# Kernel tuning notes

Measured on AMD Instinct MI355X. Metric: run time of the kernel, lower is better.

The kernel has to match this reference:

```python
import jax, jax.numpy as jnp
import numpy as np
import math

N_QUBITS = 8
N_QLAYERS = 1
LN_EPS = 1e-5


def _rx(state, theta, wire, n):
    # state: (N, 2,...,2) complex64 with n qubit axes; theta: (N,)
    sh = (theta.shape[0],) + (1,) * (n - 1)
    c = jnp.cos(theta / 2).reshape(sh)
    s = jnp.sin(theta / 2).reshape(sh)
    a = jax.lax.index_in_dim(state, 0, wire + 1, keepdims=False)
    b = jax.lax.index_in_dim(state, 1, wire + 1, keepdims=False)
    return jnp.stack([c * a - 1j * s * b, -1j * s * a + c * b], axis=wire + 1)


def _cnot(state, cw, tw, n):
    s0 = jax.lax.index_in_dim(state, 0, cw + 1, keepdims=False)
    s1 = jax.lax.index_in_dim(state, 1, cw + 1, keepdims=False)
    t_ax = tw + 1 if tw < cw else tw  # target axis index after removing control axis
    s1 = jnp.flip(s1, axis=t_ax)
    return jnp.stack([s0, s1], axis=cw + 1)


def _quantum(angles, qweights):
    # AngleEmbedding (RX) + BasicEntanglerLayers (RX + CNOT ring) + PauliZ expvals
    # angles: (N, 8) float; qweights: (1, 8) float -> returns (N, 8) float
    n = N_QUBITS
    N = angles.shape[0]
    state = jnp.zeros((N,) + (2,) * n, jnp.complex64)
    state = state.at[(slice(None),) + (0,) * n].set(1.0 + 0j)
    for w in range(n):
        state = _rx(state, angles[:, w], w, n)
    for l in range(N_QLAYERS):
        for w in range(n):
            state = _rx(state, jnp.broadcast_to(qweights[l, w], (N,)), w, n)
        for cw in range(n):
            state = _cnot(state, cw, (cw + 1) % n, n)
    probs = state.real ** 2 + state.imag ** 2
    zs = []
    for w in range(n):
        p = probs.sum(axis=tuple(a for a in range(1, n + 1) if a != w + 1))  # (N, 2)
        zs.append(p[:, 0] - p[:, 1])
    return jnp.stack(zs, axis=-1)


def _layernorm(x, g, b):
    m = x.mean(-1, keepdims=True)
    v = ((x - m) ** 2).mean(-1, keepdims=True)
    return (x - m) / jnp.sqrt(v + LN_EPS) * g + b


def _forward(x, Wq, Wk, Wv, Wo, ln1_g, ln1_b, W1, b1, W2, b2, ln2_g, ln2_b,
             ql1_w, ql1_b, qweights, ql2_w, ql2_b):
    B, S, D = x.shape
    H = 16
    dk = D // H
    q = (x @ Wq.T).reshape(B, S, H, dk)
    k = (x @ Wk.T).reshape(B, S, H, dk)
    v = (x @ Wv.T).reshape(B, S, H, dk)
    scores = jnp.einsum('bqhd,bkhd->bhqk', q, k) * (1.0 / math.sqrt(dk))
    attn = jax.nn.softmax(scores, axis=-1)
    o = jnp.einsum('bhqk,bkhd->bqhd', attn, v).reshape(B, S, D) @ Wo.T
    x = _layernorm(o + x, ln1_g, ln1_b)
    ff = jax.nn.relu(x @ W1.T + b1) @ W2.T + b2
    x = _layernorm(ff + x, ln2_g, ln2_b)
    angles = (x @ ql1_w.T + ql1_b).reshape(B * S, N_QUBITS)
    z = _quantum(angles, qweights).reshape(B, S, N_QUBITS).astype(x.dtype)
    y = jnp.concatenate([z, x], axis=2) @ ql2_w.T + ql2_b
    return y


def setup_inputs() -> dict:
    key = jax.random.key(0)
    ks = jax.random.split(key, 12)
    B, S, D, F = 4, 1024, 1024, 4096
    sc = 0.02
    w = lambda k, *sh: jax.random.normal(k, sh, jnp.float32) * sc
    return {
        'x': jax.random.normal(ks[0], (B, S, D), jnp.float32),
        'Wq': w(ks[1], D, D), 'Wk': w(ks[2], D, D), 'Wv': w(ks[3], D, D), 'Wo': w(ks[4], D, D),
        'ln1_g': jnp.ones((D,), jnp.float32), 'ln1_b': jnp.zeros((D,), jnp.float32),
        'W1': w(ks[5], F, D), 'b1': jnp.zeros((F,), jnp.float32),
        'W2': w(ks[6], D, F), 'b2': jnp.zeros((D,), jnp.float32),
        'ln2_g': jnp.ones((D,), jnp.float32), 'ln2_b': jnp.zeros((D,), jnp.float32),
        'ql1_w': w(ks[7], N_QUBITS, D), 'ql1_b': jnp.zeros((N_QUBITS,), jnp.float32),
        'qweights': jax.random.uniform(ks[8], (N_QLAYERS, N_QUBITS), jnp.float32, 0.0, 2 * np.pi),
        'ql2_w': w(ks[9], D, D + N_QUBITS), 'ql2_b': jnp.zeros((D,), jnp.float32),
    }


def reference(x, Wq, Wk, Wv, Wo, ln1_g, ln1_b, W1, b1, W2, b2, ln2_g, ln2_b,
              ql1_w, ql1_b, qweights, ql2_w, ql2_b):
    return _forward(x, Wq, Wk, Wv, Wo, ln1_g, ln1_b, W1, b1, W2, b2, ln2_g, ln2_b,
                    ql1_w, ql1_b, qweights, ql2_w, ql2_b)
```

## Files before the change

kernel.cpp:

```cpp
#include <hip/hip_runtime.h>
#include <hip/hip_bf16.h>

typedef __bf16 bf16_t;
typedef __attribute__((ext_vector_type(8))) __bf16 bf16x8;
typedef __attribute__((ext_vector_type(4))) float floatx4;

#define BM 128

enum { EPI_NONE = 0, EPI_RESID, EPI_BIAS_RELU, EPI_BIAS_RESID, EPI_QL2, EPI_PART };

__device__ __forceinline__ void gld_lds16(const bf16_t* g, bf16_t* l) {
  __builtin_amdgcn_global_load_lds(
      (__attribute__((address_space(1))) void*)(g),
      (__attribute__((address_space(3))) void*)(l), 16, 0, 0);
}

template<int ROWS, int COLS>
__device__ __forceinline__ void stage_swz(const bf16_t* g, int ld, bf16_t* lds, int tid) {
  constexpr int G = COLS / 8;
  #pragma unroll
  for (int i = 0; i < ROWS * G / 256; ++i) {
    int ci = i * 256 + tid;
    int row = ci / G, cc = ci % G;
    int gg = (G == 8) ? (cc ^ (row & 7)) : ((cc & 8) | ((cc & 7) ^ (row & 7)));
    gld_lds16(g + (size_t)row * ld + gg * 8, lds + ci * 8);
  }
}

__device__ __forceinline__ void core128(const bf16_t* __restrict__ Ag,
                                        const bf16_t* __restrict__ Bg,
                                        int Kloop, int lda, int ldb,
                                        bf16_t* As, bf16_t* Bs,
                                        floatx4 acc[4][4]) {
  const int tid = threadIdx.x;
  const int wid = tid >> 6, lane = tid & 63;
  const int wm = (wid >> 1) * 64, wn = (wid & 1) * 64;
  const int m16 = lane & 15, quad = lane >> 4;
  const int r7 = m16 & 7;
  for (int k0 = 0; k0 < Kloop; k0 += 64) {
    stage_swz<128, 64>(Ag + k0, lda, As, tid);
    stage_swz<128, 64>(Bg + k0, ldb, Bs, tid);
    __syncthreads();
    #pragma unroll
    for (int ks = 0; ks < 2; ++ks) {
      const int gi = ks * 4 + quad;
      const int slot = gi ^ r7;
      bf16x8 af[4], bfr[4];
      #pragma unroll
      for (int mt = 0; mt < 4; ++mt)
        af[mt] = *(const bf16x8*)&As[((wm + mt * 16 + m16) * 8 + slot) * 8];
      #pragma unroll
      for (int nt = 0; nt < 4; ++nt)
        bfr[nt] = *(const bf16x8*)&Bs[((wn + nt * 16 + m16) * 8 + slot) * 8];
      #pragma unroll
      for (int mt = 0; mt < 4; ++mt)
        #pragma unroll
        for (int nt = 0; nt < 4; ++nt)
          acc[mt][nt] = __builtin_amdgcn_mfma_f32_16x16x32_bf16(af[mt], bfr[nt], acc[mt][nt], 0, 0, 0);
    }
    __syncthreads();
  }
}

template<int EPI>
__global__ __launch_bounds__(256)
void gemm128(const bf16_t* __restrict__ A, const bf16_t* __restrict__ B,
             bf16_t* __restrict__ C, const float* __restrict__ bias,
             int N, int K) {
  __shared__ bf16_t As[BM * 64];
  __shared__ bf16_t Bs[BM * 64];
  const int tid = threadIdx.x;
  const int wid = tid >> 6, lane = tid & 63;
  const int wm = (wid >> 1) * 64, wn = (wid & 1) * 64;
  const int m16 = lane & 15, quad = lane >> 4;
  const int m0 = blockIdx.y * BM, n0 = blockIdx.x * BM;
  floatx4 acc[4][4];
  const floatx4 vzero = {0.f, 0.f, 0.f, 0.f};
  #pragma unroll
  for (int mt = 0; mt < 4; ++mt)
    #pragma unroll
    for (int nt = 0; nt < 4; ++nt) acc[mt][nt] = vzero;
  core128(A + (size_t)m0 * K, B + (size_t)n0 * K, K, K, K, As, Bs, acc);
  #pragma unroll
  for (int mt = 0; mt < 4; ++mt)
    #pragma unroll
    for (int nt = 0; nt < 4; ++nt) {
      const int gcol = n0 + wn + nt * 16 + m16;
      float bv = (EPI == EPI_BIAS_RELU) ? bias[gcol] : 0.f;
      #pragma unroll
      for (int r = 0; r < 4; ++r) {
        const int grow = m0 + wm + mt * 16 + quad * 4 + r;
        float v = acc[mt][nt][r];
        if (EPI == EPI_BIAS_RELU) { v += bv; v = fmaxf(v, 0.f); }
        C[(size_t)grow * N + gcol] = (bf16_t)v;
      }
    }
}

__global__ __launch_bounds__(256)
void gemm128_sk(const bf16_t* __restrict__ A, const bf16_t* __restrict__ B,
                bf16_t* __restrict__ p0, bf16_t* __restrict__ p1,
                int N, int K, int ldb, int mblocks, int nblocks) {
  __shared__ bf16_t As[BM * 64];
  __shared__ bf16_t Bs[BM * 64];
  const int tid = threadIdx.x;
  const int wid = tid >> 6, lane = tid & 63;
  const int wm = (wid >> 1) * 64, wn = (wid & 1) * 64;
  const int m16 = lane & 15, quad = lane >> 4;
  const int id = blockIdx.x;
  const int m0 = (id % mblocks) * BM;
  const int rest = id / mblocks;
  const int n0 = (rest % nblocks) * BM;
  const int kh = rest / nblocks;
  const int Keff = K / 2;
  floatx4 acc[4][4];
  const floatx4 vzero = {0.f, 0.f, 0.f, 0.f};
  #pragma unroll
  for (int mt = 0; mt < 4; ++mt)
    #pragma unroll
    for (int nt = 0; nt < 4; ++nt) acc[mt][nt] = vzero;
  core128(A + (size_t)m0 * K + (size_t)kh * Keff,
          B + (size_t)n0 * ldb + (size_t)kh * Keff, Keff, K, ldb, As, Bs, acc);
  bf16_t* Cp = kh ? p1 : p0;
  #pragma unroll
  for (int mt = 0; mt < 4; ++mt)
    #pragma unroll
    for (int nt = 0; nt < 4; ++nt) {
      const int gcol = n0 + wn + nt * 16 + m16;
      #pragma unroll
      for (int r = 0; r < 4; ++r) {
        const int grow = m0 + wm + mt * 16 + quad * 4 + r;
        Cp[(size_t)grow * N + gcol] = (bf16_t)acc[mt][nt][r];
      }
    }
}

__global__ __launch_bounds__(256)
void gemm_qkv(const bf16_t* __restrict__ X, const bf16_t* __restrict__ Wb,
              bf16_t* __restrict__ Qo, bf16_t* __restrict__ Ko, bf16_t* __restrict__ Vt) {
  __shared__ bf16_t As[BM * 64];
  __shared__ bf16_t Bs[BM * 64];
  const int tid = threadIdx.x;
  const int wid = tid >> 6, lane = tid & 63;
  const int wm = (wid >> 1) * 64, wn = (wid & 1) * 64;
  const int m16 = lane & 15, quad = lane >> 4;
  const int m0 = blockIdx.y * BM, n0 = blockIdx.x * BM;
  const int sel = blockIdx.z;
  const bf16_t* B = Wb + (size_t)sel * 1024 * 1024;
  floatx4 acc[4][4];
  const floatx4 vzero = {0.f, 0.f, 0.f, 0.f};
  #pragma unroll
  for (int mt = 0; mt < 4; ++mt)
    #pragma unroll
    for (int nt = 0; nt < 4; ++nt) acc[mt][nt] = vzero;
  core128(X + (size_t)m0 * 1024, B + (size_t)n0 * 1024, 1024, 1024, 1024, As, Bs, acc);
  if (sel < 2) {
    bf16_t* C = sel ? Ko : Qo;
    const float sc = sel ? 1.f : 0.125f;
    #pragma unroll
    for (int mt = 0; mt < 4; ++mt)
      #pragma unroll
      for (int nt = 0; nt < 4; ++nt) {
        const int gcol = n0 + wn + nt * 16 + m16;
        #pragma unroll
        for (int r = 0; r < 4; ++r) {
          const int grow = m0 + wm + mt * 16 + quad * 4 + r;
          C[(size_t)grow * 1024 + gcol] = (bf16_t)(acc[mt][nt][r] * sc);
        }
      }
  } else {
    #pragma unroll
    for (int mt = 0; mt < 4; ++mt) {
      const int grow0 = m0 + wm + mt * 16 + quad * 4;
      const int b = grow0 >> 10, s = grow0 & 1023;
      #pragma unroll
      for (int nt = 0; nt < 4; ++nt) {
        const int gcol = n0 + wn + nt * 16 + m16;
        const int h = gcol >> 6, d = gcol & 63;
        #pragma unroll
        for (int r = 0; r < 4; ++r)
          Vt[(((size_t)b * 16 + h) * 64 + d) * 1024 + s + r] = (bf16_t)acc[mt][nt][r];
      }
    }
  }
}

template<int EPI, bool OUTF32>
__global__ __launch_bounds__(256)
void gemm64(const bf16_t* __restrict__ A, const bf16_t* __restrict__ B,
            void* __restrict__ Cv,
            const bf16_t* __restrict__ resid, const float* __restrict__ bias,
            const bf16_t* __restrict__ z, const float* __restrict__ zw,
            int N, int K, int ldb, int boff, int mblocks) {
  __shared__ bf16_t As[BM * 128];
  __shared__ bf16_t Bs[64 * 128];
  const int tid = threadIdx.x;
  const int wid = tid >> 6, lane = tid & 63;
  const int wm = (wid >> 1) * 64, wn = (wid & 1) * 32;
  const int m16 = lane & 15, quad = lane >> 4;
  const int r7 = m16 & 7;
  const int id = blockIdx.x;
  const int m0 = (id % mblocks) * BM, n0 = (id / mblocks) * 64;
  const bf16_t* Ag = A + (size_t)m0 * K;
  const bf16_t* Bg = B + (size_t)n0 * ldb + boff;
  floatx4 acc[4][2];
  const floatx4 vzero = {0.f, 0.f, 0.f, 0.f};
  #pragma unroll
  for (int mt = 0; mt < 4; ++mt)
    #pragma unroll
    for (int nt = 0; nt < 2; ++nt) acc[mt][nt] = vzero;
  for (int k0 = 0; k0 < K; k0 += 128) {
    stage_swz<128, 128>(Ag + k0, K, As, tid);
    stage_swz<64, 128>(Bg + k0, ldb, Bs, tid);
    __syncthreads();
    #pragma unroll
    for (int ks = 0; ks < 4; ++ks) {
      const int gi = ks * 4 + quad;
      const int slot = (gi & 8) | ((gi & 7) ^ r7);
      bf16x8 af[4], bfr[2];
      #pragma unroll
      for (int mt = 0; mt < 4; ++mt)
        af[mt] = *(const bf16x8*)&As[((wm + mt * 16 + m16) * 16 + slot) * 8];
      #pragma unroll
      for (int nt = 0; nt < 2; ++nt)
        bfr[nt] = *(const bf16x8*)&Bs[((wn + nt * 16 + m16) * 16 + slot) * 8];
      #pragma unroll
      for (int mt = 0; mt < 4; ++mt)
        #pragma unroll
        for (int nt = 0; nt < 2; ++nt)
          acc[mt][nt] = __builtin_amdgcn_mfma_f32_16x16x32_bf16(af[mt], bfr[nt], acc[mt][nt], 0, 0, 0);
    }
    __syncthreads();
  }
  #pragma unroll
  for (int mt = 0; mt < 4; ++mt)
    #pragma unroll
    for (int nt = 0; nt < 2; ++nt) {
      const int gcol = n0 + wn + nt * 16 + m16;
      float bv = 0.f;
      if (EPI == EPI_QL2) bv = bias[gcol];
      #pragma unroll
      for (int r = 0; r < 4; ++r) {
        const int grow = m0 + wm + mt * 16 + quad * 4 + r;
        float v = acc[mt][nt][r];
        if (EPI == EPI_RESID) v += (float)resid[(size_t)grow * N + gcol];
        if (EPI == EPI_QL2) {
          float s = 0.f;
          #pragma unroll
          for (int u = 0; u < 8; ++u)
            s += (float)z[(size_t)grow * 8 + u] * zw[(size_t)gcol * 1032 + u];
          v += bv + s;
        }
        if (OUTF32) ((float*)Cv)[(size_t)grow * N + gcol] = v;
        else        ((bf16_t*)Cv)[(size_t)grow * N + gcol] = (bf16_t)v;
      }
    }
}

__global__ __launch_bounds__(256)
void attn_kernel(const bf16_t* __restrict__ Q, const bf16_t* __restrict__ Kb,
                 const bf16_t* __restrict__ Vt, bf16_t* __restrict__ O) {
  __shared__ bf16_t Qs[64 * 64];
  __shared__ bf16_t Ks[128 * 64];
  __shared__ bf16_t Vs[64 * 128];
  __shared__ bf16_t Ps[4][16 * 128];
  const int tid = threadIdx.x;
  const int wid = tid >> 6, lane = tid & 63;
  const int m16 = lane & 15, quad = lane >> 4;
  const int qt = blockIdx.x, bh = blockIdx.y;
  const int b = bh >> 4, h = bh & 15;
  const size_t qbase = ((size_t)(b * 1024 + qt * 64)) * 1024 + h * 64;
  #pragma unroll
  for (int i = 0; i < 2; ++i) {
    int ci = i * 256 + tid;
    int row = ci >> 3, cc = ci & 7;
    *(bf16x8*)&Qs[row * 64 + ((cc ^ (row & 7)) * 8)] =
        *(const bf16x8*)&Q[qbase + (size_t)row * 1024 + cc * 8];
  }
  __syncthreads();
  const int qm = wid * 16 + m16;
  bf16x8 qf0 = *(const bf16x8*)&Qs[qm * 64 + ((quad ^ (qm & 7)) * 8)];
  bf16x8 qf1 = *(const bf16x8*)&Qs[qm * 64 + (((4 + quad) ^ (qm & 7)) * 8)];
  floatx4 oacc[4];
  float rs[4];
  const floatx4 vzero = {0.f, 0.f, 0.f, 0.f};
  #pragma unroll
  for (int dt = 0; dt < 4; ++dt) oacc[dt] = vzero;
  #pragma unroll
  for (int r = 0; r < 4; ++r) rs[r] = 0.f;
  const size_t kbase = ((size_t)(b * 1024)) * 1024 + h * 64;
  const size_t vbase = ((size_t)bh * 64) * 1024;
  for (int kt = 0; kt < 8; ++kt) {
    __syncthreads();
    #pragma unroll
    for (int i = 0; i < 4; ++i) {
      int ci = i * 256 + tid;
      int row = ci >> 3, cc = ci & 7;
      *(bf16x8*)&Ks[row * 64 + ((cc ^ (row & 7)) * 8)] =
          *(const bf16x8*)&Kb[kbase + (size_t)(kt * 128 + row) * 1024 + cc * 8];
    }
    #pragma unroll
    for (int i = 0; i < 4; ++i) {
      int ci = i * 256 + tid;
      int dr = ci >> 4, cc = ci & 15;
      int gs = (cc & 8) | ((cc & 7) ^ (dr & 7));
      *(bf16x8*)&Vs[dr * 128 + gs * 8] =
          *(const bf16x8*)&Vt[vbase + (size_t)dr * 1024 + kt * 128 + cc * 8];
    }
    __syncthreads();
    floatx4 sa[8];
    #pragma unroll
    for (int nt = 0; nt < 8; ++nt) sa[nt] = vzero;
    #pragma unroll
    for (int nt = 0; nt < 8; ++nt) {
      const int n = nt * 16 + m16;
      bf16x8 kf0 = *(const bf16x8*)&Ks[n * 64 + ((quad ^ (n & 7)) * 8)];
      bf16x8 kf1 = *(const bf16x8*)&Ks[n * 64 + (((4 + quad) ^ (n & 7)) * 8)];
      sa[nt] = __builtin_amdgcn_mfma_f32_16x16x32_bf16(qf0, kf0, sa[nt], 0, 0, 0);
      sa[nt] = __builtin_amdgcn_mfma_f32_16x16x32_bf16(qf1, kf1, sa[nt], 0, 0, 0);
    }
    #pragma unroll
    for (int nt = 0; nt < 8; ++nt)
      #pragma unroll
      for (int r = 0; r < 4; ++r) {
        float pv = __expf(sa[nt][r]);
        rs[r] += pv;
        const int prow = quad * 4 + r;
        const int g = nt * 2 + (m16 >> 3);
        const int gs = (g & 8) | ((g & 7) ^ (prow & 7));
        Ps[wid][prow * 128 + gs * 8 + (m16 & 7)] = (bf16_t)pv;
      }
    bf16x8 pf[4];
    #pragma unroll
    for (int ksub = 0; ksub < 4; ++ksub) {
      const int g = ksub * 4 + quad;
      const int gs = (g & 8) | ((g & 7) ^ (m16 & 7));
      pf[ksub] = *(const bf16x8*)&Ps[wid][m16 * 128 + gs * 8];
    }
    #pragma unroll
    for (int dt = 0; dt < 4; ++dt) {
      const int n = dt * 16 + m16;
      #pragma unroll
      for (int ksub = 0; ksub < 4; ++ksub) {
        const int g = ksub * 4 + quad;
        const int gs = (g & 8) | ((g & 7) ^ (n & 7));
        bf16x8 vf = *(const bf16x8*)&Vs[n * 128 + gs * 8];
        oacc[dt] = __builtin_amdgcn_mfma_f32_16x16x32_bf16(pf[ksub], vf, oacc[dt], 0, 0, 0);
      }
    }
  }
  #pragma unroll
  for (int r = 0; r < 4; ++r) {
    rs[r] += __shfl_xor(rs[r], 1);
    rs[r] += __shfl_xor(rs[r], 2);
    rs[r] += __shfl_xor(rs[r], 4);
    rs[r] += __shfl_xor(rs[r], 8);
  }
  const size_t obase = ((size_t)(b * 1024 + qt * 64 + wid * 16)) * 1024 + h * 64;
  #pragma unroll
  for (int dt = 0; dt < 4; ++dt)
    #pragma unroll
    for (int r = 0; r < 4; ++r)
      O[obase + (size_t)(quad * 4 + r) * 1024 + dt * 16 + m16] = (bf16_t)(oacc[dt][r] / rs[r]);
}

struct Segs {
  const float* s[5];
  bf16_t* d[5];
  int n8[5];
};
__global__ __launch_bounds__(256)
void conv_multi(Segs sg) {
  const int zz = blockIdx.z;
  const float* in = sg.s[zz];
  bf16_t* out = sg.d[zz];
  const int n8 = sg.n8[zz];
  for (int i = blockIdx.x * 256 + threadIdx.x; i < n8; i += gridDim.x * 256) {
    const float* p = in + (size_t)i * 8;
    floatx4 a = *(const floatx4*)p;
    floatx4 b = *(const floatx4*)(p + 4);
    bf16x8 o;
    #pragma unroll
    for (int j = 0; j < 4; ++j) { o[j] = (bf16_t)a[j]; o[4 + j] = (bf16_t)b[j]; }
    *(bf16x8*)(out + (size_t)i * 8) = o;
  }
}

__global__ __launch_bounds__(256)
void ln_combine(const bf16_t* __restrict__ p0, const bf16_t* __restrict__ p1,
                const bf16_t* __restrict__ resid,
                const float* __restrict__ g, const float* __restrict__ b,
                bf16_t* __restrict__ out) {
  const int row = blockIdx.x * 4 + (threadIdx.x >> 6);
  const int lane = threadIdx.x & 63;
  const size_t base = (size_t)row * 1024 + lane * 16;
  bf16x8 a0 = *(const bf16x8*)&p0[base];
  bf16x8 a1 = *(const bf16x8*)&p0[base + 8];
  bf16x8 b0 = *(const bf16x8*)&p1[base];
  bf16x8 b1 = *(const bf16x8*)&p1[base + 8];
  bf16x8 c0 = *(const bf16x8*)&resid[base];
  bf16x8 c1 = *(const bf16x8*)&resid[base + 8];
  float f[16];
  #pragma unroll
  for (int j = 0; j < 8; ++j) {
    f[j]     = (float)a0[j] + (float)b0[j] + (float)c0[j];
    f[8 + j] = (float)a1[j] + (float)b1[j] + (float)c1[j];
  }
  float s = 0.f, ss = 0.f;
  #pragma unroll
  for (int j = 0; j < 16; ++j) { s += f[j]; ss += f[j] * f[j]; }
  #pragma unroll
  for (int off = 1; off < 64; off <<= 1) { s += __shfl_xor(s, off); ss += __shfl_xor(ss, off); }
  const float m = s * (1.f / 1024.f);
  const float inv_sd = rsqrtf(ss * (1.f / 1024.f) - m * m + 1e-5f);
  const float* gp = g + lane * 16;
  const float* bp = b + lane * 16;
  bf16x8 o0, o1;
  #pragma unroll
  for (int j = 0; j < 8; ++j) o0[j] = (bf16_t)((f[j] - m) * inv_sd * gp[j] + bp[j]);
  #pragma unroll
  for (int j = 0; j < 8; ++j) o1[j] = (bf16_t)((f[8 + j] - m) * inv_sd * gp[8 + j] + bp[8 + j]);
  *(bf16x8*)&out[base] = o0;
  *(bf16x8*)&out[base + 8] = o1;
}

__global__ __launch_bounds__(256)
void ln2_quantum(const bf16_t* __restrict__ p0, const bf16_t* __restrict__ p1,
                 const bf16_t* __restrict__ resid, const float* __restrict__ bias,
                 const float* __restrict__ g, const float* __restrict__ b,
                 bf16_t* __restrict__ x2,
                 const float* __restrict__ qw1, const float* __restrict__ qb1,
                 const float* __restrict__ qwt, bf16_t* __restrict__ zout,
                 const float* __restrict__ ql2w, bf16_t* __restrict__ ql2wb) {
  if (blockIdx.z == 1) {
    const int n8 = 1024 * 1032 / 8;
    for (int i = blockIdx.x * 256 + threadIdx.x; i < n8; i += gridDim.x * 256) {
      const float* p = ql2w + (size_t)i * 8;
      floatx4 a = *(const floatx4*)p;
      floatx4 bb = *(const floatx4*)(p + 4);
      bf16x8 o;
      #pragma unroll
      for (int j = 0; j < 4; ++j) { o[j] = (bf16_t)a[j]; o[4 + j] = (bf16_t)bb[j]; }
      *(bf16x8*)(ql2wb + (size_t)i * 8) = o;
    }
    return;
  }
  const int row = blockIdx.x * 4 + (threadIdx.x >> 6);
  const int lane = threadIdx.x & 63;
  const size_t base = (size_t)row * 1024 + lane * 16;
  bf16x8 a0 = *(const bf16x8*)&p0[base];
  bf16x8 a1 = *(const bf16x8*)&p0[base + 8];
  bf16x8 b0 = *(const bf16x8*)&p1[base];
  bf16x8 b1 = *(const bf16x8*)&p1[base + 8];
  bf16x8 c0 = *(const bf16x8*)&resid[base];
  bf16x8 c1 = *(const bf16x8*)&resid[base + 8];
  const float* bsp = bias + lane * 16;
  float f[16];
  #pragma unroll
  for (int j = 0; j < 8; ++j) {
    f[j]     = (float)a0[j] + (float)b0[j] + (float)c0[j] + bsp[j];
    f[8 + j] = (float)a1[j] + (float)b1[j] + (float)c1[j] + bsp[8 + j];
  }
  float s = 0.f, ss = 0.f;
  #pragma unroll
  for (int j = 0; j < 16; ++j) { s += f[j]; ss += f[j] * f[j]; }
  #pragma unroll
  for (int off = 1; off < 64; off <<= 1) { s += __shfl_xor(s, off); ss += __shfl_xor(ss, off); }
  const float m = s * (1.f / 1024.f);
  const float inv_sd = rsqrtf(ss * (1.f / 1024.f) - m * m + 1e-5f);
  const float* gp = g + lane * 16;
  const float* bp = b + lane * 16;
  bf16x8 o0, o1;
  #pragma unroll
  for (int j = 0; j < 8; ++j) o0[j] = (bf16_t)((f[j] - m) * inv_sd * gp[j] + bp[j]);
  #pragma unroll
  for (int j = 0; j < 8; ++j) o1[j] = (bf16_t)((f[8 + j] - m) * inv_sd * gp[8 + j] + bp[8 + j]);
  *(bf16x8*)&x2[base] = o0;
  *(bf16x8*)&x2[base + 8] = o1;
  float th[8];
  #pragma unroll
  for (int qq = 0; qq < 8; ++qq) {
    const float* wp = qw1 + (size_t)qq * 1024 + lane * 16;
    float sdot = 0.f;
    #pragma unroll
    for (int j = 0; j < 8; ++j)
      sdot += (float)o0[j] * wp[j] + (float)o1[j] * wp[8 + j];
    #pragma unroll
    for (int off = 1; off < 64; off <<= 1) sdot += __shfl_xor(sdot, off);
    th[qq] = sdot + qb1[qq] + qwt[qq];
  }
  if (lane == 0) {
    float c[8];
    #pragma unroll
    for (int qq = 0; qq < 8; ++qq) c[qq] = cosf(th[qq]);
    float z0 = 1.f;
    #pragma unroll
    for (int u = 1; u < 8; ++u) z0 *= c[u];
    zout[(size_t)row * 8 + 0] = (bf16_t)z0;
    float pp = c[0];
    #pragma unroll
    for (int w = 1; w < 8; ++w) { pp *= c[w]; zout[(size_t)row * 8 + w] = (bf16_t)pp; }
  }
}

extern "C" void kernel_launch(void* const* d_in, const int* in_sizes, int n_in,
                              void* d_out, int out_size, void* d_ws, size_t ws_size,
                              hipStream_t stream) {
  const float* x    = (const float*)d_in[0];
  const float* Wq   = (const float*)d_in[1];
  const float* Wk   = (const float*)d_in[2];
  const float* Wv   = (const float*)d_in[3];
  const float* Wo   = (const float*)d_in[4];
  const float* ln1g = (const float*)d_in[5];
  const float* ln1b = (const float*)d_in[6];
  const float* W1   = (const float*)d_in[7];
  const float* b1   = (const float*)d_in[8];
  const float* W2   = (const float*)d_in[9];
  const float* b2   = (const float*)d_in[10];
  const float* ln2g = (const float*)d_in[11];
  const float* ln2b = (const float*)d_in[12];
  const float* qw1  = (const float*)d_in[13];
  const float* qb1  = (const float*)d_in[14];
  const float* qwt  = (const float*)d_in[15];
  const float* ql2w = (const float*)d_in[16];
  const float* ql2b = (const float*)d_in[17];
  bf16_t* ws = (bf16_t*)d_ws;

  const size_t T = (size_t)4096 * 1024;
  const size_t M1 = (size_t)1024 * 1024;
  bf16_t* outlo = (bf16_t*)d_out;
  bf16_t* outhi = outlo + T;

  bf16_t* xb    = ws;
  bf16_t* kb    = ws + T;
  bf16_t* vt    = ws + 2 * T;
  bf16_t* ff    = ws + 3 * T;
  bf16_t* wqkvb = ff;
  bf16_t* wob   = ff + 3 * M1;
  bf16_t* w1b   = vt;
  bf16_t* w2b   = kb;
  bf16_t* ql2wb = ff;
  bf16_t* q     = outlo;
  bf16_t* o     = outhi;
  bf16_t* x1    = outhi;
  bf16_t* x2    = vt;
  bf16_t* z     = kb;

  {
    Segs sg;
    sg.s[0] = x;  sg.d[0] = xb;            sg.n8[0] = (int)(T / 8);
    sg.s[1] = Wq; sg.d[1] = wqkvb;         sg.n8[1] = (int)(M1 / 8);
    sg.s[2] = Wk; sg.d[2] = wqkvb + M1;    sg.n8[2] = (int)(M1 / 8);
    sg.s[3] = Wv; sg.d[3] = wqkvb + 2*M1;  sg.n8[3] = (int)(M1 / 8);
    sg.s[4] = Wo; sg.d[4] = wob;           sg.n8[4] = (int)(M1 / 8);
    conv_multi<<<dim3(512, 1, 5), 256, 0, stream>>>(sg);
  }
  gemm_qkv<<<dim3(8, 32, 3), 256, 0, stream>>>(xb, wqkvb, q, kb, vt);
  attn_kernel<<<dim3(16, 64), 256, 0, stream>>>(q, kb, vt, o);
  gemm128_sk<<<512, 256, 0, stream>>>(o, wob, outlo, kb, 1024, 1024, 1024, 32, 8);
  ln_combine<<<1024, 256, 0, stream>>>(outlo, kb, xb, ln1g, ln1b, x1);
  {
    Segs sg;
    sg.s[0] = W1; sg.d[0] = w1b; sg.n8[0] = (int)(T / 8);
    sg.s[1] = W2; sg.d[1] = w2b; sg.n8[1] = (int)(T / 8);
    sg.s[2] = nullptr; sg.d[2] = nullptr; sg.n8[2] = 0;
    sg.s[3] = nullptr; sg.d[3] = nullptr; sg.n8[3] = 0;
    sg.s[4] = nullptr; sg.d[4] = nullptr; sg.n8[4] = 0;
    conv_multi<<<dim3(1024, 1, 2), 256, 0, stream>>>(sg);
  }
  gemm128<EPI_BIAS_RELU><<<dim3(32, 32), 256, 0, stream>>>(x1, w1b, ff, b1, 4096, 1024);
  gemm128_sk<<<512, 256, 0, stream>>>(ff, w2b, xb, vt, 1024, 4096, 4096, 32, 8);
  ln2_quantum<<<dim3(1024, 1, 2), 256, 0, stream>>>(
      xb, vt, x1, b2, ln2g, ln2b, x2, qw1, qb1, qwt, z, ql2w, ql2wb);
  gemm64<EPI_QL2, true><<<512, 256, 0, stream>>>(
      x2, ql2wb, d_out, nullptr, ql2b, z, ql2w, 1024, 1024, 1032, 8, 32);
}
```

Measured before the change: 398.5 us.

## Double-buffer GEMM LDS staging and remap workgroups for XCD-aware tile grouping

```diff
diff --git a/kernel.cpp b/kernel.cpp
--- a/kernel.cpp
+++ b/kernel.cpp
@@ -25,6 +25,10 @@
     int gg = (G == 8) ? (cc ^ (row & 7)) : ((cc & 8) | ((cc & 7) ^ (row & 7)));
     gld_lds16(g + (size_t)row * ld + gg * 8, lds + ci * 8);
   }
+}
+
+__device__ __forceinline__ int xcd_remap(int id, int nwg) {
+  return (id & 7) * (nwg >> 3) + (id >> 3);
 }
 
 __device__ __forceinline__ void core128(const bf16_t* __restrict__ Ag,
@@ -37,10 +41,19 @@
   const int wm = (wid >> 1) * 64, wn = (wid & 1) * 64;
   const int m16 = lane & 15, quad = lane >> 4;
   const int r7 = m16 & 7;
+  constexpr int BUF = BM * 64;
+  stage_swz<128, 64>(Ag, lda, As, tid);
+  stage_swz<128, 64>(Bg, ldb, Bs, tid);
+  asm volatile("s_waitcnt vmcnt(0)" ::: "memory");
+  __syncthreads();
+  int cur = 0;
   for (int k0 = 0; k0 < Kloop; k0 += 64) {
-    stage_swz<128, 64>(Ag + k0, lda, As, tid);
-    stage_swz<128, 64>(Bg + k0, ldb, Bs, tid);
-    __syncthreads();
+    if (k0 + 64 < Kloop) {
+      stage_swz<128, 64>(Ag + k0 + 64, lda, As + (cur ^ 1) * BUF, tid);
+      stage_swz<128, 64>(Bg + k0 + 64, ldb, Bs + (cur ^ 1) * BUF, tid);
+    }
+    const bf16_t* Ab = As + cur * BUF;
+    const bf16_t* Bb = Bs + cur * BUF;
     #pragma unroll
     for (int ks = 0; ks < 2; ++ks) {
       const int gi = ks * 4 + quad;
@@ -48,17 +61,19 @@
       bf16x8 af[4], bfr[4];
       #pragma unroll
       for (int mt = 0; mt < 4; ++mt)
-        af[mt] = *(const bf16x8*)&As[((wm + mt * 16 + m16) * 8 + slot) * 8];
+        af[mt] = *(const bf16x8*)&Ab[((wm + mt * 16 + m16) * 8 + slot) * 8];
       #pragma unroll
       for (int nt = 0; nt < 4; ++nt)
-        bfr[nt] = *(const bf16x8*)&Bs[((wn + nt * 16 + m16) * 8 + slot) * 8];
+        bfr[nt] = *(const bf16x8*)&Bb[((wn + nt * 16 + m16) * 8 + slot) * 8];
       #pragma unroll
       for (int mt = 0; mt < 4; ++mt)
         #pragma unroll
         for (int nt = 0; nt < 4; ++nt)
           acc[mt][nt] = __builtin_amdgcn_mfma_f32_16x16x32_bf16(af[mt], bfr[nt], acc[mt][nt], 0, 0, 0);
     }
+    asm volatile("s_waitcnt vmcnt(0)" ::: "memory");
     __syncthreads();
+    cur ^= 1;
   }
 }
 
@@ -66,14 +81,18 @@
 __global__ __launch_bounds__(256)
 void gemm128(const bf16_t* __restrict__ A, const bf16_t* __restrict__ B,
              bf16_t* __restrict__ C, const float* __restrict__ bias,
-             int N, int K) {
-  __shared__ bf16_t As[BM * 64];
-  __shared__ bf16_t Bs[BM * 64];
+             int N, int K, int mblocks, int nblocks) {
+  __shared__ bf16_t As[2 * BM * 64];
+  __shared__ bf16_t Bs[2 * BM * 64];
   const int tid = threadIdx.x;
   const int wid = tid >> 6, lane = tid & 63;
   const int wm = (wid >> 1) * 64, wn = (wid & 1) * 64;
   const int m16 = lane & 15, quad = lane >> 4;
-  const int m0 = blockIdx.y * BM, n0 = blockIdx.x * BM;
+  const int id = xcd_remap(blockIdx.x, gridDim.x);
+  const int per_group = 8 * nblocks;
+  const int grp = id / per_group, rem = id % per_group;
+  const int m0 = (grp * 8 + (rem & 7)) * BM;
+  const int n0 = (rem >> 3) * BM;
   floatx4 acc[4][4];
   const floatx4 vzero = {0.f, 0.f, 0.f, 0.f};
   #pragma unroll
@@ -101,17 +120,20 @@
 void gemm128_sk(const bf16_t* __restrict__ A, const bf16_t* __restrict__ B,
                 bf16_t* __restrict__ p0, bf16_t* __restrict__ p1,
                 int N, int K, int ldb, int mblocks, int nblocks) {
-  __shared__ bf16_t As[BM * 64];
-  __shared__ bf16_t Bs[BM * 64];
+  __shared__ bf16_t As[2 * BM * 64];
+  __shared__ bf16_t Bs[2 * BM * 64];
   const int tid = threadIdx.x;
   const int wid = tid >> 6, lane = tid & 63;
   const int wm = (wid >> 1) * 64, wn = (wid & 1) * 64;
   const int m16 = lane & 15, quad = lane >> 4;
-  const int id = blockIdx.x;
-  const int m0 = (id % mblocks) * BM;
-  const int rest = id / mblocks;
-  const int n0 = (rest % nblocks) * BM;
-  const int kh = rest / nblocks;
+  const int id = xcd_remap(blockIdx.x, gridDim.x);
+  const int per_kh = mblocks * nblocks;
+  const int kh = id / per_kh;
+  const int rem2 = id % per_kh;
+  const int per_group = 8 * nblocks;
+  const int grp = rem2 / per_group, rem = rem2 % per_group;
+  const int m0 = (grp * 8 + (rem & 7)) * BM;
+  const int n0 = (rem >> 3) * BM;
   const int Keff = K / 2;
   floatx4 acc[4][4];
   const floatx4 vzero = {0.f, 0.f, 0.f, 0.f};
@@ -138,14 +160,19 @@
 __global__ __launch_bounds__(256)
 void gemm_qkv(const bf16_t* __restrict__ X, const bf16_t* __restrict__ Wb,
               bf16_t* __restrict__ Qo, bf16_t* __restrict__ Ko, bf16_t* __restrict__ Vt) {
-  __shared__ bf16_t As[BM * 64];
-  __shared__ bf16_t Bs[BM * 64];
+  __shared__ bf16_t As[2 * BM * 64];
+  __shared__ bf16_t Bs[2 * BM * 64];
   const int tid = threadIdx.x;
   const int wid = tid >> 6, lane = tid & 63;
   const int wm = (wid >> 1) * 64, wn = (wid & 1) * 64;
   const int m16 = lane & 15, quad = lane >> 4;
-  const int m0 = blockIdx.y * BM, n0 = blockIdx.x * BM;
-  const int sel = blockIdx.z;
+  const int id = xcd_remap(blockIdx.x, gridDim.x);
+  const int per_group = 8 * 24;
+  const int grp = id / per_group, rem = id % per_group;
+  const int m0 = (grp * 8 + (rem & 7)) * BM;
+  const int nall = rem >> 3;
+  const int n0 = (nall & 7) * BM;
+  const int sel = nall >> 3;
   const bf16_t* B = Wb + (size_t)sel * 1024 * 1024;
   floatx4 acc[4][4];
   const floatx4 vzero = {0.f, 0.f, 0.f, 0.f};
@@ -199,8 +226,12 @@
   const int wm = (wid >> 1) * 64, wn = (wid & 1) * 32;
   const int m16 = lane & 15, quad = lane >> 4;
   const int r7 = m16 & 7;
-  const int id = blockIdx.x;
-  const int m0 = (id % mblocks) * BM, n0 = (id / mblocks) * 64;
+  const int id = xcd_remap(blockIdx.x, gridDim.x);
+  const int nb_ = N >> 6;
+  const int per_group = 8 * nb_;
+  const int grp = id / per_group, rem = id % per_group;
+  const int m0 = (grp * 8 + (rem & 7)) * BM;
+  const int n0 = (rem >> 3) * 64;
   const bf16_t* Ag = A + (size_t)m0 * K;
   const bf16_t* Bg = B + (size_t)n0 * ldb + boff;
   floatx4 acc[4][2];
@@ -555,7 +586,7 @@
     sg.s[4] = Wo; sg.d[4] = wob;           sg.n8[4] = (int)(M1 / 8);
     conv_multi<<<dim3(512, 1, 5), 256, 0, stream>>>(sg);
   }
-  gemm_qkv<<<dim3(8, 32, 3), 256, 0, stream>>>(xb, wqkvb, q, kb, vt);
+  gemm_qkv<<<768, 256, 0, stream>>>(xb, wqkvb, q, kb, vt);
   attn_kernel<<<dim3(16, 64), 256, 0, stream>>>(q, kb, vt, o);
   gemm128_sk<<<512, 256, 0, stream>>>(o, wob, outlo, kb, 1024, 1024, 1024, 32, 8);
   ln_combine<<<1024, 256, 0, stream>>>(outlo, kb, xb, ln1g, ln1b, x1);
@@ -568,7 +599,7 @@
     sg.s[4] = nullptr; sg.d[4] = nullptr; sg.n8[4] = 0;
     conv_multi<<<dim3(1024, 1, 2), 256, 0, stream>>>(sg);
   }
-  gemm128<EPI_BIAS_RELU><<<dim3(32, 32), 256, 0, stream>>>(x1, w1b, ff, b1, 4096, 1024);
+  gemm128<EPI_BIAS_RELU><<<1024, 256, 0, stream>>>(x1, w1b, ff, b1, 4096, 1024, 32, 32);
   gemm128_sk<<<512, 256, 0, stream>>>(ff, w2b, xb, vt, 1024, 4096, 4096, 32, 8);
   ln2_quantum<<<dim3(1024, 1, 2), 256, 0, stream>>>(
       xb, vt, x1, b2, ln2g, ln2b, x2, qw1, qb1, qwt, z, ql2w, ql2wb);
```

Result: faster. 384.1 us (-3.6%).
